# Kernel optimization log

Measured on AMD Instinct MI355X. Metric: run time of the kernel, lower is better.

Reference implementation:

```python
import jax, jax.numpy as jnp
import numpy as np

GROUPS = 32
EPS = 1e-6


def group_norm(h, scale, bias):
    B, C, H, W = h.shape
    hg = h.reshape(B, GROUPS, -1)
    mu = hg.mean(axis=-1, keepdims=True)
    var = hg.var(axis=-1, keepdims=True)
    hg = (hg - mu) * jax.lax.rsqrt(var + EPS)
    h = hg.reshape(B, C, H, W)
    return h * scale[None, :, None, None] + bias[None, :, None, None]


def conv1x1(h, W, b):
    # 1x1 conv == per-pixel linear: (B,C,H,W) x (O,C) -> (B,O,H,W)
    return jnp.einsum('bchw,oc->bohw', h, W) + b[None, :, None, None]


def setup_inputs() -> dict:
    key = jax.random.key(0)
    ks = jax.random.split(key, 6)
    B, C, H, W = 8, 512, 64, 64
    s = 0.02
    return {
        'x': jax.random.normal(ks[0], (B, C, H, W), jnp.float32),
        'gn_scale': jnp.ones((C,), jnp.float32),
        'gn_bias': jnp.zeros((C,), jnp.float32),
        'Wq': jax.random.normal(ks[1], (C, C), jnp.float32) * s,
        'bq': jnp.zeros((C,), jnp.float32),
        'Wk': jax.random.normal(ks[2], (C, C), jnp.float32) * s,
        'bk': jnp.zeros((C,), jnp.float32),
        'Wv': jax.random.normal(ks[3], (C, C), jnp.float32) * s,
        'bv': jnp.zeros((C,), jnp.float32),
        'Wo': jax.random.normal(ks[4], (C, C), jnp.float32) * s,
        'bo': jnp.zeros((C,), jnp.float32),
    }


def reference(x, gn_scale, gn_bias, Wq, bq, Wk, bk, Wv, bv, Wo, bo):
    B, C, H, W = x.shape
    N = H * W
    h = group_norm(x, gn_scale, gn_bias)
    q = conv1x1(h, Wq, bq).reshape(B, C, N)   # (B,C,N)
    k = conv1x1(h, Wk, bk).reshape(B, C, N)
    v = conv1x1(h, Wv, bv).reshape(B, C, N)
    # scores: q^T k, scaled by C^-0.5
    w = jnp.einsum('bcq,bck->bqk', q, k) * (C ** -0.5)  # (B,N_q,N_k)
    w = jax.nn.softmax(w, axis=-1)
    # h = v @ w^T  -> (B,C,N_q)
    h = jnp.einsum('bck,bqk->bcq', v, w).reshape(B, C, H, W)
    h = conv1x1(h, Wo, bo)
    return x + h
```

## Files before the change

kernel.cpp:

```cpp
#include <hip/hip_runtime.h>
#include <math.h>

typedef __bf16 bf16_t;
typedef __bf16 bf8v __attribute__((ext_vector_type(8)));
typedef __bf16 bf4v __attribute__((ext_vector_type(4)));
typedef float  f4v  __attribute__((ext_vector_type(4)));

#define BB  8
#define CC  512
#define NN  4096
#define CPG 16
#define NCb (NN * CC)
#define WSZ (CC * CC)

#define FLG_SIZES 805306368.f
#define FLG_WS    536870912.f

__global__ void diag_out(float* out, float v) { if (threadIdx.x == 0) out[0] = v; }

__device__ __forceinline__ void gload_lds16(const bf16_t* g, bf16_t* l)
{
    __builtin_amdgcn_global_load_lds(
        (const __attribute__((address_space(1))) unsigned int*)g,
        (__attribute__((address_space(3))) unsigned int*)l, 16, 0, 0);
}

__global__ __launch_bounds__(256) void cvt_w(const float* __restrict__ a,
                                             const float* __restrict__ b,
                                             const float* __restrict__ c,
                                             const float* __restrict__ d,
                                             bf16_t* __restrict__ o)
{
    const int i = (blockIdx.x * 256 + threadIdx.x) * 4;
    const float* srcs[4] = {a, b, c, d};
#pragma unroll
    for (int m = 0; m < 4; m++) {
        float4 v = *(const float4*)(srcs[m] + i);
        bf4v w;
        w[0] = (bf16_t)v.x; w[1] = (bf16_t)v.y;
        w[2] = (bf16_t)v.z; w[3] = (bf16_t)v.w;
        *(bf4v*)(o + (size_t)m * WSZ + i) = w;
    }
}

__global__ __launch_bounds__(256) void gn_stats_part(const float* __restrict__ x,
                                                     double* __restrict__ part)
{
    const int bg = blockIdx.x >> 2;
    const int sl = blockIdx.x & 3;
    const int tid = threadIdx.x;
    const float4* xv = (const float4*)(x + (size_t)bg * CPG * NN) + sl * 4096;
    double s[4] = {0, 0, 0, 0}, ss[4] = {0, 0, 0, 0};
#pragma unroll
    for (int ii = 0; ii < 16; ii++) {
        float4 v = xv[tid + ii * 256];
        const int a = ii & 3;
        s[a]  += (double)v.x + (double)v.y + (double)v.z + (double)v.w;
        ss[a] += (double)v.x * v.x + (double)v.y * v.y
               + (double)v.z * v.z + (double)v.w * v.w;
    }
    double sT = s[0] + s[1] + s[2] + s[3];
    double ssT = ss[0] + ss[1] + ss[2] + ss[3];
    __shared__ double l1[256], l2[256];
    l1[tid] = sT; l2[tid] = ssT;
    __syncthreads();
    for (int o = 128; o > 0; o >>= 1) {
        if (tid < o) { l1[tid] += l1[tid + o]; l2[tid] += l2[tid + o]; }
        __syncthreads();
    }
    if (tid == 0) {
        part[(size_t)blockIdx.x * 2]     = l1[0];
        part[(size_t)blockIdx.x * 2 + 1] = l2[0];
    }
}

__global__ __launch_bounds__(256) void gn_stats_fin(const double* __restrict__ part,
                                                    float* __restrict__ stats)
{
    const int bg = threadIdx.x;
    double s = 0.0, ss = 0.0;
#pragma unroll
    for (int sl = 0; sl < 4; sl++) {
        s  += part[(size_t)(bg * 4 + sl) * 2];
        ss += part[(size_t)(bg * 4 + sl) * 2 + 1];
    }
    double mean = s * (1.0 / 65536.0);
    double var  = ss * (1.0 / 65536.0) - mean * mean;
    stats[bg * 2]     = (float)mean;
    stats[bg * 2 + 1] = (float)(1.0 / sqrt(var + 1e-6));
}

__global__ __launch_bounds__(256) void gn_apply_all(const float* __restrict__ x,
                                                    const float* __restrict__ gw,
                                                    const float* __restrict__ gb,
                                                    const float* __restrict__ stats,
                                                    bf16_t* __restrict__ h_all)
{
    const int b  = blockIdx.y;
    const int g  = blockIdx.x >> 4;
    const int sl = blockIdx.x & 15;
    const float* xp = x + (size_t)b * CC * NN + (size_t)g * CPG * NN;
    bf16_t* h = h_all + (size_t)b * NCb;
    const int tid = threadIdx.x;
    const float mean = stats[(b * 32 + g) * 2];
    const float rstd = stats[(b * 32 + g) * 2 + 1];
    const int cw = tid & 15;
    const float aa = rstd * gw[g * CPG + cw];
    const float bb = gb[g * CPG + cw] - mean * aa;

    __shared__ float tile[CPG][260];
    const int n0 = sl * 256;
    for (int i = tid; i < (CPG * 256) / 4; i += 256) {
        int c  = i >> 6;
        int n4 = i & 63;
        float4 v = *(const float4*)(xp + (size_t)c * NN + n0 + n4 * 4);
        tile[c][n4 * 4 + 0] = v.x;
        tile[c][n4 * 4 + 1] = v.y;
        tile[c][n4 * 4 + 2] = v.z;
        tile[c][n4 * 4 + 3] = v.w;
    }
    __syncthreads();
#pragma unroll
    for (int j = 0; j < 16; j++) {
        int n = (tid >> 4) + 16 * j;
        float v = tile[cw][n] * aa + bb;
        h[(size_t)(n0 + n) * CC + g * CPG + cw] = (bf16_t)v;
    }
}

__global__ __launch_bounds__(256) void gn_apply(const float* __restrict__ xb,
                                                const float* __restrict__ gw,
                                                const float* __restrict__ gb,
                                                const float* __restrict__ stats,
                                                bf16_t* __restrict__ h,
                                                int bg0)
{
    const int g  = blockIdx.x >> 4;
    const int sl = blockIdx.x & 15;
    const float* xp = xb + (size_t)g * CPG * NN;
    const int tid = threadIdx.x;
    const float mean = stats[(bg0 + g) * 2];
    const float rstd = stats[(bg0 + g) * 2 + 1];
    const int cw = tid & 15;
    const float aa = rstd * gw[g * CPG + cw];
    const float bb = gb[g * CPG + cw] - mean * aa;

    __shared__ float tile[CPG][260];
    const int n0 = sl * 256;
    for (int i = tid; i < (CPG * 256) / 4; i += 256) {
        int c  = i >> 6;
        int n4 = i & 63;
        float4 v = *(const float4*)(xp + (size_t)c * NN + n0 + n4 * 4);
        tile[c][n4 * 4 + 0] = v.x;
        tile[c][n4 * 4 + 1] = v.y;
        tile[c][n4 * 4 + 2] = v.z;
        tile[c][n4 * 4 + 3] = v.w;
    }
    __syncthreads();
#pragma unroll
    for (int j = 0; j < 16; j++) {
        int n = (tid >> 4) + 16 * j;
        float v = tile[cw][n] * aa + bb;
        h[(size_t)(n0 + n) * CC + g * CPG + cw] = (bf16_t)v;
    }
}

#define ABUF (128 * 32)
#define BBUF (256 * 32)
#define NBUF 3

__device__ __forceinline__ void stage_tile(
    const bf16_t* pa, const bf16_t* pb, int lda, int ldb,
    bf16_t* lA, bf16_t* lB)
{
    gload_lds16(pa,                     lA);
    gload_lds16(pa + (size_t)16 * lda,  lA + 16 * 32);
    gload_lds16(pb,                     lB);
    gload_lds16(pb + (size_t)16 * ldb,  lB + 16 * 32);
    gload_lds16(pb + (size_t)32 * ldb,  lB + 32 * 32);
    gload_lds16(pb + (size_t)48 * ldb,  lB + 48 * 32);
}

__device__ __forceinline__ void gemm_core_w(
    const bf16_t* __restrict__ A, const bf16_t* __restrict__ B,
    int K, int lda, int ldb, size_t m0, size_t n0,
    bf16_t* Asm, bf16_t* Bsm,
    int wave, int lane, int wm, int wn, int fr, int fq, f4v acc[4][8])
{
    const int gr  = lane >> 2;
    const int gcs = (((lane & 3) ^ (gr & 3)) << 3);
    const bf16_t* pa = A + (m0 + wave * 32 + gr) * lda + gcs;
    const bf16_t* pb = B + (n0 + wave * 64 + gr) * ldb + gcs;
    const int la0 = (wave * 32) * 32;
    const int lb0 = (wave * 64) * 32;
    const int fqs = ((fq ^ (fr & 3)) << 3);

    stage_tile(pa, pb, lda, ldb, Asm + la0, Bsm + lb0);
    if (K > 32)
        stage_tile(pa + 32, pb + 32, lda, ldb,
                   Asm + ABUF + la0, Bsm + BBUF + lb0);

    int buf = 0;
    for (int kt = 0; kt < K; kt += 32) {
        if (kt + 64 < K) {
            const int nb = (buf + 2 >= NBUF) ? buf + 2 - NBUF : buf + 2;
            stage_tile(pa + kt + 64, pb + kt + 64, lda, ldb,
                       Asm + nb * ABUF + la0, Bsm + nb * BBUF + lb0);
            asm volatile("s_waitcnt vmcnt(12)" ::: "memory");
        } else if (kt + 32 < K) {
            asm volatile("s_waitcnt vmcnt(6)" ::: "memory");
        } else {
            asm volatile("s_waitcnt vmcnt(0)" ::: "memory");
        }
        __builtin_amdgcn_s_barrier();

        const bf16_t* As = Asm + buf * ABUF;
        const bf16_t* Bs = Bsm + buf * BBUF;
        bf8v af[4], bfv[8];
#pragma unroll
        for (int j = 0; j < 8; j++)
            bfv[j] = *(const bf8v*)(Bs + (wn + j * 16 + fr) * 32 + fqs);
#pragma unroll
        for (int i = 0; i < 4; i++)
            af[i] = *(const bf8v*)(As + (wm + i * 16 + fr) * 32 + fqs);
#pragma unroll
        for (int i = 0; i < 4; i++)
#pragma unroll
            for (int j = 0; j < 8; j++)
                acc[i][j] = __builtin_amdgcn_mfma_f32_16x16x32_bf16(
                    af[i], bfv[j], acc[i][j], 0, 0, 0);

        __builtin_amdgcn_s_barrier();
        buf = (buf + 1 == NBUF) ? 0 : buf + 1;
    }
}

template <int MODE>
__global__ __launch_bounds__(256, 2) void gemm_bt(
    const bf16_t* __restrict__ A, const bf16_t* __restrict__ B,
    void* __restrict__ Og, const float* __restrict__ bias,
    const float* __restrict__ resid, float scale,
    int K, int lda, int ldb, int ldo)
{
    __shared__ bf16_t Asm[NBUF * ABUF];
    __shared__ bf16_t Bsm[NBUF * BBUF];
    const int tid  = threadIdx.x;
    const int lane = tid & 63, wave = tid >> 6;
    const int wm = (wave >> 1) << 6, wn = (wave & 1) << 7;
    const int fr = lane & 15, fq = lane >> 4;
    const size_t m0 = (size_t)blockIdx.x * 128, n0 = (size_t)blockIdx.y * 256;

    f4v acc[4][8];
#pragma unroll
    for (int i = 0; i < 4; i++)
#pragma unroll
        for (int j = 0; j < 8; j++) acc[i][j] = (f4v){0.f, 0.f, 0.f, 0.f};

    gemm_core_w(A, B, K, lda, ldb, m0, n0, Asm, Bsm,
                wave, lane, wm, wn, fr, fq, acc);

    if (MODE == 0) {
        bf16_t* out = (bf16_t*)Og;
#pragma unroll
        for (int i = 0; i < 4; i++) {
            const int mb = (int)m0 + wm + i * 16 + fq * 4;
#pragma unroll
            for (int j = 0; j < 8; j++) {
                const int n = (int)n0 + wn + j * 16 + fr;
                const float bn = bias ? bias[n] : 0.f;
#pragma unroll
                for (int t = 0; t < 4; t++)
                    out[(size_t)(mb + t) * ldo + n] =
                        (bf16_t)(acc[i][j][t] * scale + bn);
            }
        }
    } else {
        float* out = (float*)Og;
#pragma unroll
        for (int i = 0; i < 4; i++) {
            const int mb = (int)m0 + wm + i * 16 + fq * 4;
#pragma unroll
            for (int j = 0; j < 8; j++) {
                const int n = (int)n0 + wn + j * 16 + fr;
                const float bn = bias[n];
                float4 rq = *(const float4*)(resid + (size_t)n * ldo + mb);
                float4 o4;
                o4.x = acc[i][j][0] * scale + bn + rq.x;
                o4.y = acc[i][j][1] * scale + bn + rq.y;
                o4.z = acc[i][j][2] * scale + bn + rq.z;
                o4.w = acc[i][j][3] * scale + bn + rq.w;
                *(float4*)(out + (size_t)n * ldo + mb) = o4;
            }
        }
    }
}

__global__ __launch_bounds__(256, 2) void gemm_qkt(
    const bf16_t* __restrict__ q_all, const bf16_t* __restrict__ k_all,
    bf16_t* __restrict__ S2, int bp, float scale)
{
    __shared__ bf16_t Asm[NBUF * ABUF];
    __shared__ bf16_t Bsm[NBUF * BBUF];
    const int z = blockIdx.z;
    const bf16_t* A = q_all + (size_t)(bp + z) * NCb;
    const bf16_t* B = k_all + (size_t)(bp + z) * NCb;
    bf16_t* out = S2 + (size_t)z * NN * NN;

    const int tid  = threadIdx.x;
    const int lane = tid & 63, wave = tid >> 6;
    const int wm = (wave >> 1) << 6, wn = (wave & 1) << 7;
    const int fr = lane & 15, fq = lane >> 4;
    const size_t m0 = (size_t)blockIdx.x * 128, n0 = (size_t)blockIdx.y * 256;

    f4v acc[4][8];
#pragma unroll
    for (int i = 0; i < 4; i++)
#pragma unroll
        for (int j = 0; j < 8; j++) acc[i][j] = (f4v){0.f, 0.f, 0.f, 0.f};

    gemm_core_w(A, B, 512, 512, 512, m0, n0, Asm, Bsm,
                wave, lane, wm, wn, fr, fq, acc);

#pragma unroll
    for (int i = 0; i < 4; i++) {
        const int mb = (int)m0 + wm + i * 16 + fq * 4;
#pragma unroll
        for (int j = 0; j < 8; j++) {
            const int n = (int)n0 + wn + j * 16 + fr;
#pragma unroll
            for (int t = 0; t < 4; t++)
                out[(size_t)(mb + t) * NN + n] = (bf16_t)(acc[i][j][t] * scale);
        }
    }
}

__global__ __launch_bounds__(256, 2) void gemm_pv2(
    const bf16_t* __restrict__ S2, const bf16_t* __restrict__ v_all,
    float* __restrict__ P, int bp)
{
    __shared__ bf16_t Asm[NBUF * ABUF];
    __shared__ bf16_t Bsm[NBUF * BBUF];
    const int slot = blockIdx.z >> 2;
    const int s    = blockIdx.z & 3;
    const int k0   = s * 1024;
    const bf16_t* A = S2 + (size_t)slot * NN * NN + k0;
    const bf16_t* B = v_all + (size_t)(bp + slot) * NCb + k0;
    float* out = P + ((size_t)slot * 4 + s) * NCb;

    const int tid  = threadIdx.x;
    const int lane = tid & 63, wave = tid >> 6;
    const int wm = (wave >> 1) << 6, wn = (wave & 1) << 7;
    const int fr = lane & 15, fq = lane >> 4;
    const size_t m0 = (size_t)blockIdx.x * 128, n0 = (size_t)blockIdx.y * 256;

    f4v acc[4][8];
#pragma unroll
    for (int i = 0; i < 4; i++)
#pragma unroll
        for (int j = 0; j < 8; j++) acc[i][j] = (f4v){0.f, 0.f, 0.f, 0.f};

    gemm_core_w(A, B, 1024, NN, NN, m0, n0, Asm, Bsm,
                wave, lane, wm, wn, fr, fq, acc);

#pragma unroll
    for (int i = 0; i < 4; i++) {
        const int mb = (int)m0 + wm + i * 16 + fq * 4;
#pragma unroll
        for (int j = 0; j < 8; j++) {
            const int n = (int)n0 + wn + j * 16 + fr;
#pragma unroll
            for (int t = 0; t < 4; t++)
                out[(size_t)(mb + t) * CC + n] = acc[i][j][t];
        }
    }
}

__global__ __launch_bounds__(256) void pv_reduce2(const float* __restrict__ P,
                                                  bf16_t* __restrict__ O_all,
                                                  int bp)
{
    const int slot = blockIdx.y;
    const size_t i = ((size_t)blockIdx.x * 256 + threadIdx.x) * 4;
    const float* Ps = P + (size_t)slot * 4 * NCb;
    float4 sv = *(const float4*)(Ps + i);
#pragma unroll
    for (int z = 1; z < 4; z++) {
        float4 t = *(const float4*)(Ps + (size_t)z * NCb + i);
        sv.x += t.x; sv.y += t.y; sv.z += t.z; sv.w += t.w;
    }
    bf4v o;
    o[0] = (bf16_t)sv.x; o[1] = (bf16_t)sv.y;
    o[2] = (bf16_t)sv.z; o[3] = (bf16_t)sv.w;
    *(bf4v*)(O_all + (size_t)(bp + slot) * NCb + i) = o;
}

__global__ __launch_bounds__(256, 2) void gemm_pv_split(
    const bf16_t* __restrict__ A, const bf16_t* __restrict__ B,
    float* __restrict__ P, int KS)
{
    __shared__ bf16_t Asm[NBUF * ABUF];
    __shared__ bf16_t Bsm[NBUF * BBUF];
    const int tid  = threadIdx.x;
    const int lane = tid & 63, wave = tid >> 6;
    const int wm = (wave >> 1) << 6, wn = (wave & 1) << 7;
    const int fr = lane & 15, fq = lane >> 4;
    const size_t m0 = (size_t)blockIdx.x * 128, n0 = (size_t)blockIdx.y * 256;
    const int z  = blockIdx.z;
    const int k0 = z * KS;

    f4v acc[4][8];
#pragma unroll
    for (int i = 0; i < 4; i++)
#pragma unroll
        for (int j = 0; j < 8; j++) acc[i][j] = (f4v){0.f, 0.f, 0.f, 0.f};

    gemm_core_w(A + k0, B + k0, KS, NN, NN, m0, n0, Asm, Bsm,
                wave, lane, wm, wn, fr, fq, acc);

    float* out = P + (size_t)z * NCb;
#pragma unroll
    for (int i = 0; i < 4; i++) {
        const int mb = (int)m0 + wm + i * 16 + fq * 4;
#pragma unroll
        for (int j = 0; j < 8; j++) {
            const int n = (int)n0 + wn + j * 16 + fr;
#pragma unroll
            for (int t = 0; t < 4; t++)
                out[(size_t)(mb + t) * CC + n] = acc[i][j][t];
        }
    }
}

__global__ __launch_bounds__(256) void pv_reduce(const float* __restrict__ P,
                                                 bf16_t* __restrict__ O, int NS)
{
    const size_t i = ((size_t)blockIdx.x * 256 + threadIdx.x) * 4;
    float4 s = *(const float4*)(P + i);
    for (int z = 1; z < NS; z++) {
        float4 t = *(const float4*)(P + (size_t)z * NCb + i);
        s.x += t.x; s.y += t.y; s.z += t.z; s.w += t.w;
    }
    bf4v o;
    o[0] = (bf16_t)s.x; o[1] = (bf16_t)s.y;
    o[2] = (bf16_t)s.z; o[3] = (bf16_t)s.w;
    *(bf4v*)(O + i) = o;
}

__global__ __launch_bounds__(256, 2) void gemm_out_all(
    const bf16_t* __restrict__ Oall, const bf16_t* __restrict__ Wo,
    float* __restrict__ outg, const float* __restrict__ bo,
    const float* __restrict__ x)
{
    __shared__ bf16_t Asm[NBUF * ABUF];
    __shared__ bf16_t Bsm[NBUF * BBUF];
    const int b = blockIdx.z;
    const bf16_t* A = Oall + (size_t)b * NCb;
    float* out = outg + (size_t)b * CC * NN;
    const float* resid = x + (size_t)b * CC * NN;

    const int tid  = threadIdx.x;
    const int lane = tid & 63, wave = tid >> 6;
    const int wm = (wave >> 1) << 6, wn = (wave & 1) << 7;
    const int fr = lane & 15, fq = lane >> 4;
    const size_t m0 = (size_t)blockIdx.x * 128, n0 = (size_t)blockIdx.y * 256;

    f4v acc[4][8];
#pragma unroll
    for (int i = 0; i < 4; i++)
#pragma unroll
        for (int j = 0; j < 8; j++) acc[i][j] = (f4v){0.f, 0.f, 0.f, 0.f};

    gemm_core_w(A, Wo, 512, 512, 512, m0, n0, Asm, Bsm,
                wave, lane, wm, wn, fr, fq, acc);

#pragma unroll
    for (int i = 0; i < 4; i++) {
        const int mb = (int)m0 + wm + i * 16 + fq * 4;
#pragma unroll
        for (int j = 0; j < 8; j++) {
            const int n = (int)n0 + wn + j * 16 + fr;
            const float bn = bo[n];
            float4 rq = *(const float4*)(resid + (size_t)n * NN + mb);
            float4 o4;
            o4.x = acc[i][j][0] + bn + rq.x;
            o4.y = acc[i][j][1] + bn + rq.y;
            o4.z = acc[i][j][2] + bn + rq.z;
            o4.w = acc[i][j][3] + bn + rq.w;
            *(float4*)(out + (size_t)n * NN + mb) = o4;
        }
    }
}

__global__ __launch_bounds__(256, 2) void gemm_qkv_all(
    const bf16_t* __restrict__ h_all, const bf16_t* __restrict__ Wb,
    const float* __restrict__ bq, const float* __restrict__ bk,
    const float* __restrict__ bv,
    bf16_t* __restrict__ q_all, bf16_t* __restrict__ k_all,
    bf16_t* __restrict__ v_all)
{
    __shared__ bf16_t Asm[NBUF * ABUF];
    __shared__ bf16_t Bsm[NBUF * BBUF];
    const int sel = blockIdx.z >> 3;
    const int b   = blockIdx.z & 7;
    const bf16_t* h = h_all + (size_t)b * NCb;
    const bf16_t* B = Wb + (size_t)sel * WSZ;
    const float* bias = (sel == 0) ? bq : (sel == 1) ? bk : bv;
    bf16_t* out = ((sel == 0) ? q_all : (sel == 1) ? k_all : v_all)
                + (size_t)b * NCb;

    const int tid  = threadIdx.x;
    const int lane = tid & 63, wave = tid >> 6;
    const int wm = (wave >> 1) << 6, wn = (wave & 1) << 7;
    const int fr = lane & 15, fq = lane >> 4;
    const size_t m0 = (size_t)blockIdx.x * 128, n0 = (size_t)blockIdx.y * 256;

    f4v acc[4][8];
#pragma unroll
    for (int i = 0; i < 4; i++)
#pragma unroll
        for (int j = 0; j < 8; j++) acc[i][j] = (f4v){0.f, 0.f, 0.f, 0.f};

    gemm_core_w(h, B, 512, 512, 512, m0, n0, Asm, Bsm,
                wave, lane, wm, wn, fr, fq, acc);

    if (sel < 2) {
#pragma unroll
        for (int i = 0; i < 4; i++) {
            const int mb = (int)m0 + wm + i * 16 + fq * 4;
#pragma unroll
            for (int j = 0; j < 8; j++) {
                const int n = (int)n0 + wn + j * 16 + fr;
                const float bn = bias[n];
#pragma unroll
                for (int t = 0; t < 4; t++)
                    out[(size_t)(mb + t) * 512 + n] =
                        (bf16_t)(acc[i][j][t] + bn);
            }
        }
    } else {
#pragma unroll
        for (int i = 0; i < 4; i++) {
            const int mb = (int)m0 + wm + i * 16 + fq * 4;
#pragma unroll
            for (int j = 0; j < 8; j++) {
                const int n = (int)n0 + wn + j * 16 + fr;
                const float bn = bias[n];
                bf4v pk;
#pragma unroll
                for (int t = 0; t < 4; t++)
                    pk[t] = (bf16_t)(acc[i][j][t] + bn);
                *(bf4v*)(out + (size_t)n * NN + mb) = pk;
            }
        }
    }
}

__global__ __launch_bounds__(256, 2) void gemm_qkv(
    const bf16_t* __restrict__ h, const bf16_t* __restrict__ Wb,
    const float* __restrict__ bq, const float* __restrict__ bk,
    const float* __restrict__ bv,
    bf16_t* __restrict__ q, bf16_t* __restrict__ k, bf16_t* __restrict__ v)
{
    __shared__ bf16_t Asm[NBUF * ABUF];
    __shared__ bf16_t Bsm[NBUF * BBUF];
    const int z = blockIdx.z;
    const bf16_t* B = Wb + (size_t)z * WSZ;
    const float* bias = (z == 0) ? bq : (z == 1) ? bk : bv;
    bf16_t* out = (z == 0) ? q : (z == 1) ? k : v;

    const int tid  = threadIdx.x;
    const int lane = tid & 63, wave = tid >> 6;
    const int wm = (wave >> 1) << 6, wn = (wave & 1) << 7;
    const int fr = lane & 15, fq = lane >> 4;
    const size_t m0 = (size_t)blockIdx.x * 128, n0 = (size_t)blockIdx.y * 256;

    f4v acc[4][8];
#pragma unroll
    for (int i = 0; i < 4; i++)
#pragma unroll
        for (int j = 0; j < 8; j++) acc[i][j] = (f4v){0.f, 0.f, 0.f, 0.f};

    gemm_core_w(h, B, 512, 512, 512, m0, n0, Asm, Bsm,
                wave, lane, wm, wn, fr, fq, acc);

    if (z < 2) {
#pragma unroll
        for (int i = 0; i < 4; i++) {
            const int mb = (int)m0 + wm + i * 16 + fq * 4;
#pragma unroll
            for (int j = 0; j < 8; j++) {
                const int n = (int)n0 + wn + j * 16 + fr;
                const float bn = bias[n];
#pragma unroll
                for (int t = 0; t < 4; t++)
                    out[(size_t)(mb + t) * 512 + n] =
                        (bf16_t)(acc[i][j][t] + bn);
            }
        }
    } else {
#pragma unroll
        for (int i = 0; i < 4; i++) {
            const int mb = (int)m0 + wm + i * 16 + fq * 4;
#pragma unroll
            for (int j = 0; j < 8; j++) {
                const int n = (int)n0 + wn + j * 16 + fr;
                const float bn = bias[n];
                bf4v pk;
#pragma unroll
                for (int t = 0; t < 4; t++)
                    pk[t] = (bf16_t)(acc[i][j][t] + bn);
                *(bf4v*)(out + (size_t)n * NN + mb) = pk;
            }
        }
    }
}

__global__ __launch_bounds__(256) void softmax_kernel(bf16_t* __restrict__ S)
{
    const int wave = threadIdx.x >> 6, lane = threadIdx.x & 63;
    const size_t row = (size_t)blockIdx.x * 4 + wave;
    bf16_t* p = S + row * NN;
    float f[64];
    float mx = -1e30f;
#pragma unroll
    for (int c = 0; c < 8; c++) {
        bf8v v = ((const bf8v*)p)[c * 64 + lane];
#pragma unroll
        for (int j = 0; j < 8; j++) {
            f[c * 8 + j] = (float)v[j];
            mx = fmaxf(mx, f[c * 8 + j]);
        }
    }
#pragma unroll
    for (int off = 32; off > 0; off >>= 1) mx = fmaxf(mx, __shfl_xor(mx, off));
    float sum = 0.f;
#pragma unroll
    for (int i = 0; i < 64; i++) { f[i] = expf(f[i] - mx); sum += f[i]; }
#pragma unroll
    for (int off = 32; off > 0; off >>= 1) sum += __shfl_xor(sum, off);
    const float inv = 1.f / sum;
#pragma unroll
    for (int c = 0; c < 8; c++) {
        bf8v o;
#pragma unroll
        for (int j = 0; j < 8; j++) o[j] = (bf16_t)(f[c * 8 + j] * inv);
        ((bf8v*)p)[c * 64 + lane] = o;
    }
}

extern "C" void kernel_launch(void* const* d_in, const int* in_sizes, int n_in,
                              void* d_out, int out_size, void* d_ws, size_t ws_size,
                              hipStream_t stream)
{
    const float* x  = (const float*)d_in[0];
    const float* gw = (const float*)d_in[1];
    const float* gb = (const float*)d_in[2];
    const float* Wq = (const float*)d_in[3];
    const float* bq = (const float*)d_in[4];
    const float* Wk = (const float*)d_in[5];
    const float* bk = (const float*)d_in[6];
    const float* Wv = (const float*)d_in[7];
    const float* bv = (const float*)d_in[8];
    const float* Wo = (const float*)d_in[9];
    const float* bo = (const float*)d_in[10];
    float* out = (float*)d_out;

    bool ok = (n_in == 11) && (out_size == BB * CC * NN) &&
              (in_sizes[0] == BB * CC * NN) &&
              (in_sizes[1] == CC) && (in_sizes[2] == CC) &&
              (in_sizes[3] == WSZ) && (in_sizes[4] == CC) &&
              (in_sizes[5] == WSZ) && (in_sizes[6] == CC) &&
              (in_sizes[7] == WSZ) && (in_sizes[8] == CC) &&
              (in_sizes[9] == WSZ) && (in_sizes[10] == CC);
    if (!ok) { diag_out<<<dim3(1), 64, 0, stream>>>(out, FLG_SIZES); return; }

    const float sc = 0.044194173824159216f;

    bf16_t* Wb    = (bf16_t*)d_ws;
    float*  stats = (float*)(Wb + (size_t)4 * WSZ);
    double* part  = (double*)(stats + 1024);
    bf16_t* base  = (bf16_t*)(part + 2048);
    const size_t head = (size_t)4 * WSZ * 2 + 1024 * 4 + 2048 * 8;

    const size_t sfull = (size_t)NN * NN * 2;

    cvt_w<<<dim3(256), 256, 0, stream>>>(Wq, Wk, Wv, Wo, Wb);
    gn_stats_part<<<dim3(1024), 256, 0, stream>>>(x, part);
    gn_stats_fin<<<dim3(1), 256, 0, stream>>>(part, stats);

    if (ws_size >= head + (size_t)4 * BB * NCb * 2 + 2 * sfull) {
        bf16_t* h_all = base;
        bf16_t* q_all = h_all + (size_t)BB * NCb;
        bf16_t* k_all = q_all + (size_t)BB * NCb;
        bf16_t* v_all = k_all + (size_t)BB * NCb;
        bf16_t* S2    = v_all + (size_t)BB * NCb;
        float*  P     = out;
        bf16_t* O_all = h_all;

        gn_apply_all<<<dim3(512, 8), 256, 0, stream>>>(x, gw, gb, stats, h_all);
        gemm_qkv_all<<<dim3(32, 2, 24), 256, 0, stream>>>(
            h_all, Wb, bq, bk, bv, q_all, k_all, v_all);

        for (int bp = 0; bp < BB; bp += 2) {
            gemm_qkt<<<dim3(32, 16, 2), 256, 0, stream>>>(
                q_all, k_all, S2, bp, sc);
            softmax_kernel<<<dim3(2 * NN / 4), 256, 0, stream>>>(S2);
            gemm_pv2<<<dim3(32, 2, 8), 256, 0, stream>>>(S2, v_all, P, bp);
            pv_reduce2<<<dim3(NCb / 1024, 2), 256, 0, stream>>>(P, O_all, bp);
        }

        gemm_out_all<<<dim3(32, 2, 8), 256, 0, stream>>>(
            O_all, Wb + (size_t)3 * WSZ, out, bo, x);
        return;
    }

    bf16_t* h = base;
    bf16_t* q = h + (size_t)NCb;
    bf16_t* k = q + (size_t)NCb;
    bf16_t* v = k + (size_t)NCb;
    bf16_t* S = v + (size_t)NCb;
    bf16_t* O = h;
    const size_t fixed = head + (size_t)4 * NCb * 2;

    if (ws_size < fixed + (size_t)128 * NN * 2) {
        diag_out<<<dim3(1), 64, 0, stream>>>(out, FLG_WS); return;
    }

    int NS = 0;
    if (ws_size >= fixed + sfull + (size_t)8 * NCb * 4)      NS = 8;
    else if (ws_size >= fixed + sfull + (size_t)4 * NCb * 4) NS = 4;
    else if (ws_size >= fixed + sfull + (size_t)2 * NCb * 4) NS = 2;

    if (NS) {
        float* P = (float*)(S + (size_t)NN * NN);
        for (int b = 0; b < BB; b++) {
            const float* xb   = x   + (size_t)b * CC * NN;
            float*       outb = out + (size_t)b * CC * NN;

            gn_apply<<<dim3(512), 256, 0, stream>>>(xb, gw, gb, stats, h, b * 32);
            gemm_qkv<<<dim3(32, 2, 3), 256, 0, stream>>>(h, Wb, bq, bk, bv, q, k, v);

            gemm_bt<0><<<dim3(32, 16), 256, 0, stream>>>(
                q, k, S, nullptr, nullptr, sc, 512, 512, 512, 4096);
            softmax_kernel<<<dim3(NN / 4), 256, 0, stream>>>(S);

            gemm_pv_split<<<dim3(32, 2, NS), 256, 0, stream>>>(S, v, P, NN / NS);
            pv_reduce<<<dim3(NCb / 1024), 256, 0, stream>>>(P, O, NS);

            gemm_bt<2><<<dim3(32, 2), 256, 0, stream>>>(
                O, Wb + (size_t)3 * WSZ, outb, bo, xb, 1.f,
                512, 512, 512, 4096);
        }
        return;
    }

    int CH = 128;
    while (CH < NN && fixed + (size_t)(CH * 2) * NN * 2 <= ws_size) CH *= 2;

    for (int b = 0; b < BB; b++) {
        const float* xb   = x   + (size_t)b * CC * NN;
        float*       outb = out + (size_t)b * CC * NN;

        gn_apply<<<dim3(512), 256, 0, stream>>>(xb, gw, gb, stats, h, b * 32);
        gemm_qkv<<<dim3(32, 2, 3), 256, 0, stream>>>(h, Wb, bq, bk, bv, q, k, v);

        for (int r0 = 0; r0 < NN; r0 += CH) {
            gemm_bt<0><<<dim3(CH / 128, 16), 256, 0, stream>>>(
                q + (size_t)r0 * CC, k, S, nullptr, nullptr, sc,
                512, 512, 512, 4096);
            softmax_kernel<<<dim3(CH / 4), 256, 0, stream>>>(S);
            gemm_bt<0><<<dim3(CH / 128, 2), 256, 0, stream>>>(
                S, v, O + (size_t)r0 * CC, nullptr, nullptr, 1.f,
                4096, 4096, 4096, 512);
        }

        gemm_bt<2><<<dim3(32, 2), 256, 0, stream>>>(
            O, Wb + (size_t)3 * WSZ, outb, bo, xb, 1.f,
            512, 512, 512, 4096);
    }
}
```

Baseline: 811.0 us.

## Switch main-path GEMMs to 256x256 tiles with 8-wave eight-slot LDS pipeline

Adds a new GEMM core in which 512 threads (8 waves) compute a 256x256 output tile. It stages 32-wide K slices through eight swizzled LDS slots using direct global-to-LDS loads, interleaved with 16x16x32 bf16 MFMA bursts at raised wave priority. The QKV, QK^T, PV and output projection kernels on the main path now use this core with half as many blocks. The aim is more data reuse per tile and better overlap of loads with MFMA. In exchange it uses 128KB of LDS per block, adds many barriers and larger accumulators per thread, and leaves fewer blocks to spread across the CUs.

```diff
diff --git a/kernel.cpp b/kernel.cpp
--- a/kernel.cpp
+++ b/kernel.cpp
@@ -295,16 +295,18 @@
     }
 }
 
-__global__ __launch_bounds__(256, 2) void gemm_qkt(
-    const bf16_t* __restrict__ q_all, const bf16_t* __restrict__ k_all,
-    bf16_t* __restrict__ S2, int bp, float scale)
+__global__ __launch_bounds__(256, 2) void gemm_qkv(
+    const bf16_t* __restrict__ h, const bf16_t* __restrict__ Wb,
+    const float* __restrict__ bq, const float* __restrict__ bk,
+    const float* __restrict__ bv,
+    bf16_t* __restrict__ q, bf16_t* __restrict__ k, bf16_t* __restrict__ v)
 {
     __shared__ bf16_t Asm[NBUF * ABUF];
     __shared__ bf16_t Bsm[NBUF * BBUF];
     const int z = blockIdx.z;
-    const bf16_t* A = q_all + (size_t)(bp + z) * NCb;
-    const bf16_t* B = k_all + (size_t)(bp + z) * NCb;
-    bf16_t* out = S2 + (size_t)z * NN * NN;
+    const bf16_t* B = Wb + (size_t)z * WSZ;
+    const float* bias = (z == 0) ? bq : (z == 1) ? bk : bv;
+    bf16_t* out = (z == 0) ? q : (z == 1) ? k : v;
 
     const int tid  = threadIdx.x;
     const int lane = tid & 63, wave = tid >> 6;
@@ -318,80 +320,39 @@
 #pragma unroll
         for (int j = 0; j < 8; j++) acc[i][j] = (f4v){0.f, 0.f, 0.f, 0.f};
 
-    gemm_core_w(A, B, 512, 512, 512, m0, n0, Asm, Bsm,
+    gemm_core_w(h, B, 512, 512, 512, m0, n0, Asm, Bsm,
                 wave, lane, wm, wn, fr, fq, acc);
 
-#pragma unroll
-    for (int i = 0; i < 4; i++) {
-        const int mb = (int)m0 + wm + i * 16 + fq * 4;
-#pragma unroll
-        for (int j = 0; j < 8; j++) {
-            const int n = (int)n0 + wn + j * 16 + fr;
-#pragma unroll
-            for (int t = 0; t < 4; t++)
-                out[(size_t)(mb + t) * NN + n] = (bf16_t)(acc[i][j][t] * scale);
-        }
-    }
-}
-
-__global__ __launch_bounds__(256, 2) void gemm_pv2(
-    const bf16_t* __restrict__ S2, const bf16_t* __restrict__ v_all,
-    float* __restrict__ P, int bp)
-{
-    __shared__ bf16_t Asm[NBUF * ABUF];
-    __shared__ bf16_t Bsm[NBUF * BBUF];
-    const int slot = blockIdx.z >> 2;
-    const int s    = blockIdx.z & 3;
-    const int k0   = s * 1024;
-    const bf16_t* A = S2 + (size_t)slot * NN * NN + k0;
-    const bf16_t* B = v_all + (size_t)(bp + slot) * NCb + k0;
-    float* out = P + ((size_t)slot * 4 + s) * NCb;
-
-    const int tid  = threadIdx.x;
-    const int lane = tid & 63, wave = tid >> 6;
-    const int wm = (wave >> 1) << 6, wn = (wave & 1) << 7;
-    const int fr = lane & 15, fq = lane >> 4;
-    const size_t m0 = (size_t)blockIdx.x * 128, n0 = (size_t)blockIdx.y * 256;
-
-    f4v acc[4][8];
-#pragma unroll
-    for (int i = 0; i < 4; i++)
-#pragma unroll
-        for (int j = 0; j < 8; j++) acc[i][j] = (f4v){0.f, 0.f, 0.f, 0.f};
-
-    gemm_core_w(A, B, 1024, NN, NN, m0, n0, Asm, Bsm,
-                wave, lane, wm, wn, fr, fq, acc);
-
-#pragma unroll
-    for (int i = 0; i < 4; i++) {
-        const int mb = (int)m0 + wm + i * 16 + fq * 4;
-#pragma unroll
-        for (int j = 0; j < 8; j++) {
-            const int n = (int)n0 + wn + j * 16 + fr;
-#pragma unroll
-            for (int t = 0; t < 4; t++)
-                out[(size_t)(mb + t) * CC + n] = acc[i][j][t];
-        }
-    }
-}
-
-__global__ __launch_bounds__(256) void pv_reduce2(const float* __restrict__ P,
-                                                  bf16_t* __restrict__ O_all,
-                                                  int bp)
-{
-    const int slot = blockIdx.y;
-    const size_t i = ((size_t)blockIdx.x * 256 + threadIdx.x) * 4;
-    const float* Ps = P + (size_t)slot * 4 * NCb;
-    float4 sv = *(const float4*)(Ps + i);
-#pragma unroll
-    for (int z = 1; z < 4; z++) {
-        float4 t = *(const float4*)(Ps + (size_t)z * NCb + i);
-        sv.x += t.x; sv.y += t.y; sv.z += t.z; sv.w += t.w;
-    }
-    bf4v o;
-    o[0] = (bf16_t)sv.x; o[1] = (bf16_t)sv.y;
-    o[2] = (bf16_t)sv.z; o[3] = (bf16_t)sv.w;
-    *(bf4v*)(O_all + (size_t)(bp + slot) * NCb + i) = o;
+    if (z < 2) {
+#pragma unroll
+        for (int i = 0; i < 4; i++) {
+            const int mb = (int)m0 + wm + i * 16 + fq * 4;
+#pragma unroll
+            for (int j = 0; j < 8; j++) {
+                const int n = (int)n0 + wn + j * 16 + fr;
+                const float bn = bias[n];
+#pragma unroll
+                for (int t = 0; t < 4; t++)
+                    out[(size_t)(mb + t) * 512 + n] =
+                        (bf16_t)(acc[i][j][t] + bn);
+            }
+        }
+    } else {
+#pragma unroll
+        for (int i = 0; i < 4; i++) {
+            const int mb = (int)m0 + wm + i * 16 + fq * 4;
+#pragma unroll
+            for (int j = 0; j < 8; j++) {
+                const int n = (int)n0 + wn + j * 16 + fr;
+                const float bn = bias[n];
+                bf4v pk;
+#pragma unroll
+                for (int t = 0; t < 4; t++)
+                    pk[t] = (bf16_t)(acc[i][j][t] + bn);
+                *(bf4v*)(out + (size_t)n * NN + mb) = pk;
+            }
+        }
+    }
 }
 
 __global__ __launch_bounds__(256, 2) void gemm_pv_split(
@@ -446,173 +407,328 @@
     *(bf4v*)(O + i) = o;
 }
 
-__global__ __launch_bounds__(256, 2) void gemm_out_all(
-    const bf16_t* __restrict__ Oall, const bf16_t* __restrict__ Wo,
-    float* __restrict__ outg, const float* __restrict__ bo,
-    const float* __restrict__ x)
-{
-    __shared__ bf16_t Asm[NBUF * ABUF];
-    __shared__ bf16_t Bsm[NBUF * BBUF];
-    const int b = blockIdx.z;
-    const bf16_t* A = Oall + (size_t)b * NCb;
-    float* out = outg + (size_t)b * CC * NN;
-    const float* resid = x + (size_t)b * CC * NN;
-
+#define SL8 8192
+
+__device__ __forceinline__ void stage_g(const bf16_t* g, int ld, bf16_t* slot,
+                                        int r0, int srow, int schk)
+{
+    gload_lds16(g + (size_t)(r0 + srow) * ld + schk,      slot + r0 * 32);
+    gload_lds16(g + (size_t)(r0 + 16 + srow) * ld + schk, slot + (r0 + 16) * 32);
+}
+
+__device__ __forceinline__ void rd4(bf8v* dst, const bf16_t* slot, int base,
+                                    int fr, int rchk)
+{
+#pragma unroll
+    for (int i = 0; i < 4; i++)
+        dst[i] = *(const bf8v*)(slot + (base + i * 16 + fr) * 32 + rchk);
+}
+
+template <int IH>
+__device__ __forceinline__ void mma16(const bf8v* af, const bf8v* bfv,
+                                      f4v (&acc)[8][4])
+{
+    __builtin_amdgcn_s_setprio(1);
+#pragma unroll
+    for (int i = 0; i < 4; i++)
+#pragma unroll
+        for (int j = 0; j < 4; j++)
+            acc[IH * 4 + i][j] = __builtin_amdgcn_mfma_f32_16x16x32_bf16(
+                af[i], bfv[j], acc[IH * 4 + i][j], 0, 0, 0);
+    __builtin_amdgcn_s_setprio(0);
+}
+
+#define FENCE8 asm volatile("" ::: "memory")
+#define BAR8   do { FENCE8; __builtin_amdgcn_s_barrier(); FENCE8; } while (0)
+
+__device__ __forceinline__ void gemm_core8(
+    const bf16_t* __restrict__ A, const bf16_t* __restrict__ B,
+    int K, int lda, int ldb, size_t m0, size_t n0,
+    bf16_t* lds, f4v (&acc)[8][4])
+{
     const int tid  = threadIdx.x;
     const int lane = tid & 63, wave = tid >> 6;
-    const int wm = (wave >> 1) << 6, wn = (wave & 1) << 7;
+    const int wm2 = wave >> 2, wn4 = wave & 3;
     const int fr = lane & 15, fq = lane >> 4;
-    const size_t m0 = (size_t)blockIdx.x * 128, n0 = (size_t)blockIdx.y * 256;
-
-    f4v acc[4][8];
-#pragma unroll
-    for (int i = 0; i < 4; i++)
-#pragma unroll
-        for (int j = 0; j < 8; j++) acc[i][j] = (f4v){0.f, 0.f, 0.f, 0.f};
-
-    gemm_core_w(A, Wo, 512, 512, 512, m0, n0, Asm, Bsm,
-                wave, lane, wm, wn, fr, fq, acc);
-
-#pragma unroll
-    for (int i = 0; i < 4; i++) {
-        const int mb = (int)m0 + wm + i * 16 + fq * 4;
-#pragma unroll
-        for (int j = 0; j < 8; j++) {
-            const int n = (int)n0 + wn + j * 16 + fr;
-            const float bn = bo[n];
-            float4 rq = *(const float4*)(resid + (size_t)n * NN + mb);
-            float4 o4;
-            o4.x = acc[i][j][0] + bn + rq.x;
-            o4.y = acc[i][j][1] + bn + rq.y;
-            o4.z = acc[i][j][2] + bn + rq.z;
-            o4.w = acc[i][j][3] + bn + rq.w;
-            *(float4*)(out + (size_t)n * NN + mb) = o4;
-        }
-    }
-}
-
-__global__ __launch_bounds__(256, 2) void gemm_qkv_all(
+    const int srow = lane >> 2;
+    const int schk = ((lane & 3) ^ (srow & 3)) << 3;
+    const int r0   = wave * 32;
+    const int rchk = ((fq ^ (fr & 3)) << 3);
+
+    const bf16_t* Ag = A + m0 * lda;
+    const bf16_t* Bg = B + n0 * ldb;
+    const int NT = K >> 6;
+
+    bf16_t* S0 = lds;
+    bf16_t* S1 = lds + 1 * SL8;
+    bf16_t* S2 = lds + 2 * SL8;
+    bf16_t* S3 = lds + 3 * SL8;
+    bf16_t* S4 = lds + 4 * SL8;
+    bf16_t* S5 = lds + 5 * SL8;
+    bf16_t* S6 = lds + 6 * SL8;
+    bf16_t* S7 = lds + 7 * SL8;
+
+    const int abase = wm2 * 128;
+    const int bbase = wn4 * 64;
+
+    stage_g(Ag,      lda, S0, r0, srow, schk);
+    stage_g(Ag + 32, lda, S1, r0, srow, schk);
+    stage_g(Bg,      ldb, S2, r0, srow, schk);
+    stage_g(Bg + 32, ldb, S3, r0, srow, schk);
+    stage_g(Bg + 64, ldb, S6, r0, srow, schk);
+    stage_g(Ag + 64, lda, S4, r0, srow, schk);
+    stage_g(Bg + 96, ldb, S7, r0, srow, schk);
+    asm volatile("s_waitcnt vmcnt(6)" ::: "memory");
+    __builtin_amdgcn_s_barrier();
+    FENCE8;
+
+    bf8v af[4], bfv[4];
+    const int iters = NT >> 1;
+    for (int it = 0; it < iters; it++) {
+        const int t1k = (2 * it + 1) << 6;
+        const int t2k = (2 * it + 2) << 6;
+        const int t3k = (2 * it + 3) << 6;
+        const bool s23 = (2 * it + 2) < NT;
+
+        rd4(af, S0, abase, fr, rchk);
+        rd4(bfv, S2, bbase, fr, rchk);
+        stage_g(Ag + t1k + 32, lda, S5, r0, srow, schk);
+        BAR8; mma16<0>(af, bfv, acc); BAR8;
+
+        rd4(af, S0, abase + 64, fr, rchk);
+        if (s23) stage_g(Bg + t2k, ldb, S2, r0, srow, schk);
+        BAR8; mma16<1>(af, bfv, acc); BAR8;
+
+        rd4(af, S1, abase, fr, rchk);
+        rd4(bfv, S3, bbase, fr, rchk);
+        if (s23) stage_g(Ag + t2k, lda, S0, r0, srow, schk);
+        BAR8; mma16<0>(af, bfv, acc); BAR8;
+
+        rd4(af, S1, abase + 64, fr, rchk);
+        if (s23) {
+            stage_g(Bg + t2k + 32, ldb, S3, r0, srow, schk);
+            asm volatile("s_waitcnt vmcnt(6)" ::: "memory");
+        } else {
+            asm volatile("s_waitcnt vmcnt(0)" ::: "memory");
+        }
+        BAR8; mma16<1>(af, bfv, acc); BAR8;
+
+        rd4(af, S4, abase, fr, rchk);
+        rd4(bfv, S6, bbase, fr, rchk);
+        if (s23) stage_g(Ag + t2k + 32, lda, S1, r0, srow, schk);
+        BAR8; mma16<0>(af, bfv, acc); BAR8;
+
+        rd4(af, S4, abase + 64, fr, rchk);
+        if (s23) stage_g(Bg + t3k, ldb, S6, r0, srow, schk);
+        BAR8; mma16<1>(af, bfv, acc); BAR8;
+
+        rd4(af, S5, abase, fr, rchk);
+        rd4(bfv, S7, bbase, fr, rchk);
+        if (s23) stage_g(Ag + t3k, lda, S4, r0, srow, schk);
+        BAR8; mma16<0>(af, bfv, acc); BAR8;
+
+        rd4(af, S5, abase + 64, fr, rchk);
+        if (s23) {
+            stage_g(Bg + t3k + 32, ldb, S7, r0, srow, schk);
+            asm volatile("s_waitcnt vmcnt(6)" ::: "memory");
+        } else {
+            asm volatile("s_waitcnt vmcnt(0)" ::: "memory");
+        }
+        BAR8; mma16<1>(af, bfv, acc); BAR8;
+    }
+}
+
+__global__ __launch_bounds__(512, 2) void gemm_qkv_all8(
     const bf16_t* __restrict__ h_all, const bf16_t* __restrict__ Wb,
     const float* __restrict__ bq, const float* __restrict__ bk,
     const float* __restrict__ bv,
     bf16_t* __restrict__ q_all, bf16_t* __restrict__ k_all,
     bf16_t* __restrict__ v_all)
 {
-    __shared__ bf16_t Asm[NBUF * ABUF];
-    __shared__ bf16_t Bsm[NBUF * BBUF];
+    __shared__ bf16_t lds8[8 * SL8];
     const int sel = blockIdx.z >> 3;
     const int b   = blockIdx.z & 7;
-    const bf16_t* h = h_all + (size_t)b * NCb;
+    const bf16_t* A = h_all + (size_t)b * NCb;
     const bf16_t* B = Wb + (size_t)sel * WSZ;
     const float* bias = (sel == 0) ? bq : (sel == 1) ? bk : bv;
     bf16_t* out = ((sel == 0) ? q_all : (sel == 1) ? k_all : v_all)
                 + (size_t)b * NCb;
-
-    const int tid  = threadIdx.x;
-    const int lane = tid & 63, wave = tid >> 6;
-    const int wm = (wave >> 1) << 6, wn = (wave & 1) << 7;
+    const size_t m0 = (size_t)blockIdx.x * 256, n0 = (size_t)blockIdx.y * 256;
+
+    f4v acc[8][4];
+#pragma unroll
+    for (int i = 0; i < 8; i++)
+#pragma unroll
+        for (int j = 0; j < 4; j++) acc[i][j] = (f4v){0.f, 0.f, 0.f, 0.f};
+
+    gemm_core8(A, B, 512, 512, 512, m0, n0, lds8, acc);
+
+    const int lane = threadIdx.x & 63, wave = threadIdx.x >> 6;
+    const int wm2 = wave >> 2, wn4 = wave & 3;
     const int fr = lane & 15, fq = lane >> 4;
-    const size_t m0 = (size_t)blockIdx.x * 128, n0 = (size_t)blockIdx.y * 256;
-
-    f4v acc[4][8];
-#pragma unroll
-    for (int i = 0; i < 4; i++)
-#pragma unroll
-        for (int j = 0; j < 8; j++) acc[i][j] = (f4v){0.f, 0.f, 0.f, 0.f};
-
-    gemm_core_w(h, B, 512, 512, 512, m0, n0, Asm, Bsm,
-                wave, lane, wm, wn, fr, fq, acc);
 
     if (sel < 2) {
 #pragma unroll
-        for (int i = 0; i < 4; i++) {
-            const int mb = (int)m0 + wm + i * 16 + fq * 4;
-#pragma unroll
-            for (int j = 0; j < 8; j++) {
-                const int n = (int)n0 + wn + j * 16 + fr;
+        for (int ig = 0; ig < 8; ig++) {
+            const int mb = (int)m0 + wm2 * 128 + ig * 16 + fq * 4;
+#pragma unroll
+            for (int j = 0; j < 4; j++) {
+                const int n = (int)n0 + wn4 * 64 + j * 16 + fr;
                 const float bn = bias[n];
 #pragma unroll
                 for (int t = 0; t < 4; t++)
                     out[(size_t)(mb + t) * 512 + n] =
-                        (bf16_t)(acc[i][j][t] + bn);
+                        (bf16_t)(acc[ig][j][t] + bn);
             }
         }
     } else {
 #pragma unroll
-        for (int i = 0; i < 4; i++) {
-            const int mb = (int)m0 + wm + i * 16 + fq * 4;
-#pragma unroll
-            for (int j = 0; j < 8; j++) {
-                const int n = (int)n0 + wn + j * 16 + fr;
+        for (int ig = 0; ig < 8; ig++) {
+            const int mb = (int)m0 + wm2 * 128 + ig * 16 + fq * 4;
+#pragma unroll
+            for (int j = 0; j < 4; j++) {
+                const int n = (int)n0 + wn4 * 64 + j * 16 + fr;
                 const float bn = bias[n];
                 bf4v pk;
 #pragma unroll
                 for (int t = 0; t < 4; t++)
-                    pk[t] = (bf16_t)(acc[i][j][t] + bn);
+                    pk[t] = (bf16_t)(acc[ig][j][t] + bn);
                 *(bf4v*)(out + (size_t)n * NN + mb) = pk;
             }
         }
     }
 }
 
-__global__ __launch_bounds__(256, 2) void gemm_qkv(
-    const bf16_t* __restrict__ h, const bf16_t* __restrict__ Wb,
-    const float* __restrict__ bq, const float* __restrict__ bk,
-    const float* __restrict__ bv,
-    bf16_t* __restrict__ q, bf16_t* __restrict__ k, bf16_t* __restrict__ v)
-{
-    __shared__ bf16_t Asm[NBUF * ABUF];
-    __shared__ bf16_t Bsm[NBUF * BBUF];
+__global__ __launch_bounds__(512, 2) void gemm_qkt8(
+    const bf16_t* __restrict__ q_all, const bf16_t* __restrict__ k_all,
+    bf16_t* __restrict__ S2b, int bp, float scale)
+{
+    __shared__ bf16_t lds8[8 * SL8];
     const int z = blockIdx.z;
-    const bf16_t* B = Wb + (size_t)z * WSZ;
-    const float* bias = (z == 0) ? bq : (z == 1) ? bk : bv;
-    bf16_t* out = (z == 0) ? q : (z == 1) ? k : v;
-
-    const int tid  = threadIdx.x;
-    const int lane = tid & 63, wave = tid >> 6;
-    const int wm = (wave >> 1) << 6, wn = (wave & 1) << 7;
+    const bf16_t* A = q_all + (size_t)(bp + z) * NCb;
+    const bf16_t* B = k_all + (size_t)(bp + z) * NCb;
+    bf16_t* out = S2b + (size_t)z * NN * NN;
+    const size_t m0 = (size_t)blockIdx.x * 256, n0 = (size_t)blockIdx.y * 256;
+
+    f4v acc[8][4];
+#pragma unroll
+    for (int i = 0; i < 8; i++)
+#pragma unroll
+        for (int j = 0; j < 4; j++) acc[i][j] = (f4v){0.f, 0.f, 0.f, 0.f};
+
+    gemm_core8(A, B, 512, 512, 512, m0, n0, lds8, acc);
+
+    const int lane = threadIdx.x & 63, wave = threadIdx.x >> 6;
+    const int wm2 = wave >> 2, wn4 = wave & 3;
     const int fr = lane & 15, fq = lane >> 4;
-    const size_t m0 = (size_t)blockIdx.x * 128, n0 = (size_t)blockIdx.y * 256;
-
-    f4v acc[4][8];
-#pragma unroll
-    for (int i = 0; i < 4; i++)
-#pragma unroll
-        for (int j = 0; j < 8; j++) acc[i][j] = (f4v){0.f, 0.f, 0.f, 0.f};
-
-    gemm_core_w(h, B, 512, 512, 512, m0, n0, Asm, Bsm,
-                wave, lane, wm, wn, fr, fq, acc);
-
-    if (z < 2) {
-#pragma unroll
-        for (int i = 0; i < 4; i++) {
-            const int mb = (int)m0 + wm + i * 16 + fq * 4;
-#pragma unroll
-            for (int j = 0; j < 8; j++) {
-                const int n = (int)n0 + wn + j * 16 + fr;
-                const float bn = bias[n];
-#pragma unroll
-                for (int t = 0; t < 4; t++)
-                    out[(size_t)(mb + t) * 512 + n] =
-                        (bf16_t)(acc[i][j][t] + bn);
-            }
-        }
-    } else {
-#pragma unroll
-        for (int i = 0; i < 4; i++) {
-            const int mb = (int)m0 + wm + i * 16 + fq * 4;
-#pragma unroll
-            for (int j = 0; j < 8; j++) {
-                const int n = (int)n0 + wn + j * 16 + fr;
-                const float bn = bias[n];
-                bf4v pk;
-#pragma unroll
-                for (int t = 0; t < 4; t++)
-                    pk[t] = (bf16_t)(acc[i][j][t] + bn);
-                *(bf4v*)(out + (size_t)n * NN + mb) = pk;
-            }
-        }
-    }
+#pragma unroll
+    for (int ig = 0; ig < 8; ig++) {
+        const int mb = (int)m0 + wm2 * 128 + ig * 16 + fq * 4;
+#pragma unroll
+        for (int j = 0; j < 4; j++) {
+            const int n = (int)n0 + wn4 * 64 + j * 16 + fr;
+#pragma unroll
+            for (int t = 0; t < 4; t++)
+                out[(size_t)(mb + t) * NN + n] = (bf16_t)(acc[ig][j][t] * scale);
+        }
+    }
+}
+
+__global__ __launch_bounds__(512, 2) void gemm_pv28(
+    const bf16_t* __restrict__ S2b, const bf16_t* __restrict__ v_all,
+    float* __restrict__ P, int bp)
+{
+    __shared__ bf16_t lds8[8 * SL8];
+    const int slot = blockIdx.z >> 2;
+    const int s    = blockIdx.z & 3;
+    const int k0   = s * 1024;
+    const bf16_t* A = S2b + (size_t)slot * NN * NN + k0;
+    const bf16_t* B = v_all + (size_t)(bp + slot) * NCb + k0;
+    float* out = P + ((size_t)slot * 4 + s) * NCb;
+    const size_t m0 = (size_t)blockIdx.x * 256, n0 = (size_t)blockIdx.y * 256;
+
+    f4v acc[8][4];
+#pragma unroll
+    for (int i = 0; i < 8; i++)
+#pragma unroll
+        for (int j = 0; j < 4; j++) acc[i][j] = (f4v){0.f, 0.f, 0.f, 0.f};
+
+    gemm_core8(A, B, 1024, NN, NN, m0, n0, lds8, acc);
+
+    const int lane = threadIdx.x & 63, wave = threadIdx.x >> 6;
+    const int wm2 = wave >> 2, wn4 = wave & 3;
+    const int fr = lane & 15, fq = lane >> 4;
+#pragma unroll
+    for (int ig = 0; ig < 8; ig++) {
+        const int mb = (int)m0 + wm2 * 128 + ig * 16 + fq * 4;
+#pragma unroll
+        for (int j = 0; j < 4; j++) {
+            const int n = (int)n0 + wn4 * 64 + j * 16 + fr;
+#pragma unroll
+            for (int t = 0; t < 4; t++)
+                out[(size_t)(mb + t) * CC + n] = acc[ig][j][t];
+        }
+    }
+}
+
+__global__ __launch_bounds__(512, 2) void gemm_out_all8(
+    const bf16_t* __restrict__ Oall, const bf16_t* __restrict__ Wo,
+    float* __restrict__ outg, const float* __restrict__ bo,
+    const float* __restrict__ x)
+{
+    __shared__ bf16_t lds8[8 * SL8];
+    const int b = blockIdx.z;
+    const bf16_t* A = Oall + (size_t)b * NCb;
+    float* out = outg + (size_t)b * CC * NN;
+    const float* resid = x + (size_t)b * CC * NN;
+    const size_t m0 = (size_t)blockIdx.x * 256, n0 = (size_t)blockIdx.y * 256;
+
+    f4v acc[8][4];
+#pragma unroll
+    for (int i = 0; i < 8; i++)
+#pragma unroll
+        for (int j = 0; j < 4; j++) acc[i][j] = (f4v){0.f, 0.f, 0.f, 0.f};
+
+    gemm_core8(A, Wo, 512, 512, 512, m0, n0, lds8, acc);
+
+    const int lane = threadIdx.x & 63, wave = threadIdx.x >> 6;
+    const int wm2 = wave >> 2, wn4 = wave & 3;
+    const int fr = lane & 15, fq = lane >> 4;
+#pragma unroll
+    for (int ig = 0; ig < 8; ig++) {
+        const int mb = (int)m0 + wm2 * 128 + ig * 16 + fq * 4;
+#pragma unroll
+        for (int j = 0; j < 4; j++) {
+            const int n = (int)n0 + wn4 * 64 + j * 16 + fr;
+            const float bn = bo[n];
+            float4 rq = *(const float4*)(resid + (size_t)n * NN + mb);
+            float4 o4;
+            o4.x = acc[ig][j][0] + bn + rq.x;
+            o4.y = acc[ig][j][1] + bn + rq.y;
+            o4.z = acc[ig][j][2] + bn + rq.z;
+            o4.w = acc[ig][j][3] + bn + rq.w;
+            *(float4*)(out + (size_t)n * NN + mb) = o4;
+        }
+    }
+}
+
+__global__ __launch_bounds__(256) void pv_reduce2(const float* __restrict__ P,
+                                                  bf16_t* __restrict__ O_all,
+                                                  int bp)
+{
+    const int slot = blockIdx.y;
+    const size_t i = ((size_t)blockIdx.x * 256 + threadIdx.x) * 4;
+    const float* Ps = P + (size_t)slot * 4 * NCb;
+    float4 sv = *(const float4*)(Ps + i);
+#pragma unroll
+    for (int z = 1; z < 4; z++) {
+        float4 t = *(const float4*)(Ps + (size_t)z * NCb + i);
+        sv.x += t.x; sv.y += t.y; sv.z += t.z; sv.w += t.w;
+    }
+    bf4v o;
+    o[0] = (bf16_t)sv.x; o[1] = (bf16_t)sv.y;
+    o[2] = (bf16_t)sv.z; o[3] = (bf16_t)sv.w;
+    *(bf4v*)(O_all + (size_t)(bp + slot) * NCb + i) = o;
 }
 
 __global__ __launch_bounds__(256) void softmax_kernel(bf16_t* __restrict__ S)
@@ -698,18 +814,18 @@
         bf16_t* O_all = h_all;
 
         gn_apply_all<<<dim3(512, 8), 256, 0, stream>>>(x, gw, gb, stats, h_all);
-        gemm_qkv_all<<<dim3(32, 2, 24), 256, 0, stream>>>(
+        gemm_qkv_all8<<<dim3(16, 2, 24), 512, 0, stream>>>(
             h_all, Wb, bq, bk, bv, q_all, k_all, v_all);
 
         for (int bp = 0; bp < BB; bp += 2) {
-            gemm_qkt<<<dim3(32, 16, 2), 256, 0, stream>>>(
+            gemm_qkt8<<<dim3(16, 16, 2), 512, 0, stream>>>(
                 q_all, k_all, S2, bp, sc);
             softmax_kernel<<<dim3(2 * NN / 4), 256, 0, stream>>>(S2);
-            gemm_pv2<<<dim3(32, 2, 8), 256, 0, stream>>>(S2, v_all, P, bp);
+            gemm_pv28<<<dim3(16, 2, 8), 512, 0, stream>>>(S2, v_all, P, bp);
             pv_reduce2<<<dim3(NCb / 1024, 2), 256, 0, stream>>>(P, O_all, bp);
         }
 
-        gemm_out_all<<<dim3(32, 2, 8), 256, 0, stream>>>(
+        gemm_out_all8<<<dim3(16, 2, 8), 512, 0, stream>>>(
             O_all, Wb + (size_t)3 * WSZ, out, bo, x);
         return;
     }
```

New measurement: 754.0 us. -7.0%, faster.
